# Kernel optimization log

Measured on AMD Instinct MI355X. Metric: run time of the kernel, lower is better.

Reference implementation:

```python
import jax, jax.numpy as jnp
import numpy as np

B, N, C = 2, 10000, 128
NH, NP = 4, 20          # n_heads, n_points (n_levels = 1)
DH = C // NH            # head dim = 32
HW = 100                # spatial shape (100, 100), N = HW*HW


def setup_inputs() -> dict:
    key = jax.random.key(0)
    ks = jax.random.split(key, 12)
    s = 0.05  # small param scale so softmax/linears stay well-conditioned
    return {
        "query": jax.random.normal(ks[0], (B, N, C), jnp.float32),
        "query_pos": jax.random.normal(ks[1], (B, N, C), jnp.float32),
        "W_val": jax.random.normal(ks[2], (C, C), jnp.float32) * s,
        "b_val": jax.random.normal(ks[3], (C,), jnp.float32) * s,
        "W_off": jax.random.normal(ks[4], (NH * NP * 2, C), jnp.float32) * s,
        "b_off": jax.random.normal(ks[5], (NH * NP * 2,), jnp.float32) * s,
        "W_attn": jax.random.normal(ks[6], (NH * NP, C), jnp.float32) * s,
        "b_attn": jax.random.normal(ks[7], (NH * NP,), jnp.float32) * s,
        "W_out1": jax.random.normal(ks[8], (C, C), jnp.float32) * s,
        "b_out1": jax.random.normal(ks[9], (C,), jnp.float32) * s,
        "W_out2": jax.random.normal(ks[10], (C, C), jnp.float32) * s,
        "b_out2": jax.random.normal(ks[11], (C,), jnp.float32) * s,
    }


def _msdeform_forward(query, query_pos, W_val, b_val, W_off, b_off,
                      W_attn, b_attn, W_out1, b_out1, W_out2, b_out2):
    residual = query
    q = query + query_pos  # pos added; value branch also uses q (query.clone())

    # reference points: meshgrid of (z, x) normalized to (0,1), shape (N, 2)
    lin = (jnp.arange(HW, dtype=jnp.float32) + 0.5) / HW
    ref_z, ref_x = jnp.meshgrid(lin, lin, indexing="ij")
    ref = jnp.stack([ref_z.reshape(-1), ref_x.reshape(-1)], axis=-1)  # (N,2)

    # projections
    value = (q @ W_val.T + b_val).reshape(B, N, NH, DH).transpose(0, 2, 1, 3)  # (B,NH,N,DH)
    off = (q @ W_off.T + b_off).reshape(B, N, NH, NP, 2)
    attn = jax.nn.softmax((q @ W_attn.T + b_attn).reshape(B, N, NH, NP), axis=-1)

    # sampling locations in normalized coords; offset normalizer = (W, H) = (100, 100)
    loc = ref[None, :, None, None, :] + off / HW  # (B,N,NH,NP,2)

    # grid_sample bilinear, align_corners=False, zeros padding:
    # pixel coord = loc * size - 0.5
    x = (loc[..., 0] * HW - 0.5).transpose(0, 2, 1, 3)  # (B,NH,N,NP)
    y = (loc[..., 1] * HW - 0.5).transpose(0, 2, 1, 3)
    aw = attn.transpose(0, 2, 1, 3)                     # (B,NH,N,NP)

    x0f = jnp.floor(x); y0f = jnp.floor(y)
    wx1 = x - x0f; wy1 = y - y0f
    wx0 = 1.0 - wx1; wy0 = 1.0 - wy1
    ix0 = x0f.astype(jnp.int32); iy0 = y0f.astype(jnp.int32)
    ix1 = ix0 + 1; iy1 = iy0 + 1

    def gather(ix, iy):
        valid = ((ix >= 0) & (ix < HW) & (iy >= 0) & (iy < HW)).astype(value.dtype)
        idx = jnp.clip(iy, 0, HW - 1) * HW + jnp.clip(ix, 0, HW - 1)  # (B,NH,N,NP)
        g = jnp.take_along_axis(value, idx.reshape(B, NH, N * NP, 1), axis=2)
        return g.reshape(B, NH, N, NP, DH) * valid[..., None]

    sampled = ((wx0 * wy0)[..., None] * gather(ix0, iy0)
               + (wx1 * wy0)[..., None] * gather(ix1, iy0)
               + (wx0 * wy1)[..., None] * gather(ix0, iy1)
               + (wx1 * wy1)[..., None] * gather(ix1, iy1))  # (B,NH,N,NP,DH)

    out = (sampled * aw[..., None]).sum(axis=3)             # (B,NH,N,DH)
    out = out.transpose(0, 2, 1, 3).reshape(B, N, C)
    out = out @ W_out1.T + b_out1   # MSDeformAttn.output_proj
    out = out @ W_out2.T + b_out2   # wrapper output_proj
    return out + residual           # dropout is identity in eval


def reference(query, query_pos, W_val, b_val, W_off, b_off,
              W_attn, b_attn, W_out1, b_out1, W_out2, b_out2):
    return _msdeform_forward(query, query_pos, W_val, b_val, W_off, b_off,
                             W_attn, b_attn, W_out1, b_out1, W_out2, b_out2)
```

## Files before the change

### kernel.cpp

```cpp
#include <hip/hip_runtime.h>
#include <hip/hip_bf16.h>
#include <math.h>

#define NTOK 10000
#define BATCH 2
#define CDIM 128
#define NHEAD 4
#define NPNT 20
#define DHEAD 32
#define HWDIM 100
#define MROWS (BATCH * NTOK)
#define OPAD 384
#define PTOK 8
#define PHALO 4
#define PDIM 16
#define NPATCH 13
#define CELLPAD 40

typedef __attribute__((ext_vector_type(8))) short short8v;
typedef __attribute__((ext_vector_type(4))) short short4v;
typedef __attribute__((ext_vector_type(4))) float f32x4;

__device__ __forceinline__ float asf(unsigned u) {
  union { unsigned u; float f; } c; c.u = u; return c.f;
}

__device__ __forceinline__ void acc_cell(const __hip_bfloat16* p, float w,
                                         f32x4& a0, f32x4& a1) {
  int4 u = *(const int4*)p;
  f32x4 g0, g1;
  g0.x = asf(((unsigned)u.x) << 16); g0.y = asf(((unsigned)u.x) & 0xFFFF0000u);
  g0.z = asf(((unsigned)u.y) << 16); g0.w = asf(((unsigned)u.y) & 0xFFFF0000u);
  g1.x = asf(((unsigned)u.z) << 16); g1.y = asf(((unsigned)u.z) & 0xFFFF0000u);
  g1.z = asf(((unsigned)u.w) << 16); g1.w = asf(((unsigned)u.w) & 0xFFFF0000u);
  a0 += g0 * w;
  a1 += g1 * w;
}

__global__ __launch_bounds__(128) void prep_kernel(
    const float* __restrict__ W_val, const float* __restrict__ b_val,
    const float* __restrict__ W_off, const float* __restrict__ b_off,
    const float* __restrict__ W_attn, const float* __restrict__ b_attn,
    const float* __restrict__ W1, const float* __restrict__ b1,
    const float* __restrict__ W2, const float* __restrict__ b2,
    __hip_bfloat16* __restrict__ Wcat, float* __restrict__ bcat,
    __hip_bfloat16* __restrict__ Wc_bf, float* __restrict__ bc) {
  __shared__ float w2row[128];
  __shared__ float red[128];
  const int blk = blockIdx.x, c = threadIdx.x;
  if (blk < OPAD) {
    float v = 0.f, bv = 0.f;
    if (blk < 128) {
      v = W_val[blk * 128 + c]; bv = b_val[blk];
    } else {
      int h = (blk - 128) >> 6, k = (blk - 128) & 63;
      if (k < 40) { v = W_off[(h * 40 + k) * 128 + c]; bv = b_off[h * 40 + k]; }
      else if (k < 60) { v = W_attn[(h * 20 + k - 40) * 128 + c]; bv = b_attn[h * 20 + k - 40]; }
    }
    Wcat[(size_t)blk * 128 + c] = __float2bfloat16(v);
    if (c == 0) bcat[blk] = bv;
  } else {
    const int o = blk - OPAD;
    w2row[c] = W2[o * 128 + c];
    __syncthreads();
    float acc = 0.f;
    for (int k = 0; k < 128; ++k) acc += w2row[k] * W1[k * 128 + c];
    Wc_bf[(size_t)o * 128 + c] = __float2bfloat16(acc);
    red[c] = w2row[c] * b1[c];
    __syncthreads();
    for (int s = 64; s > 0; s >>= 1) {
      if (c < s) red[c] += red[c + s];
      __syncthreads();
    }
    if (c == 0) bc[o] = b2[o] + red[0];
  }
}

__global__ __launch_bounds__(256) void proj1_kernel(
    const float* __restrict__ query, const float* __restrict__ qpos,
    const __hip_bfloat16* __restrict__ Wcat, const float* __restrict__ bcat,
    __hip_bfloat16* __restrict__ value, __hip_bfloat16* __restrict__ oa) {
  __shared__ __hip_bfloat16 qa[64][128];
  __shared__ __hip_bfloat16 wb[64][128];
  const int t = threadIdx.x;
  const int r0 = blockIdx.x * 64;

#pragma unroll
  for (int i = 0; i < 4; ++i) {
    int lin = t + 256 * i;
    int r = lin >> 4, g = lin & 15;
    int c = g << 3;
    float4 v0 = make_float4(0.f, 0.f, 0.f, 0.f);
    float4 v1 = make_float4(0.f, 0.f, 0.f, 0.f);
    if (r0 + r < MROWS) {
      const float* p = query + (size_t)(r0 + r) * CDIM + c;
      v0 = *(const float4*)p;
      v1 = *(const float4*)(p + 4);
      const float* p2 = qpos + (size_t)(r0 + r) * CDIM + c;
      float4 u0 = *(const float4*)p2;
      float4 u1 = *(const float4*)(p2 + 4);
      v0.x += u0.x; v0.y += u0.y; v0.z += u0.z; v0.w += u0.w;
      v1.x += u1.x; v1.y += u1.y; v1.z += u1.z; v1.w += u1.w;
    }
    __hip_bfloat16* dst = &qa[r][(g ^ (r & 7)) << 3];
    dst[0] = __float2bfloat16(v0.x); dst[1] = __float2bfloat16(v0.y);
    dst[2] = __float2bfloat16(v0.z); dst[3] = __float2bfloat16(v0.w);
    dst[4] = __float2bfloat16(v1.x); dst[5] = __float2bfloat16(v1.y);
    dst[6] = __float2bfloat16(v1.z); dst[7] = __float2bfloat16(v1.w);
  }
  {
    const int ot = blockIdx.y * 192;
#pragma unroll
    for (int i = 0; i < 4; ++i) {
      int lin = t + 256 * i;
      int r = lin >> 4, g = lin & 15;
      short8v w = *(const short8v*)(Wcat + (size_t)(ot + r) * 128 + (g << 3));
      *(short8v*)&wb[r][(g ^ (r & 7)) << 3] = w;
    }
  }
  __syncthreads();

  const int wid = t >> 6;
  const int lane = t & 63;
  const int wr = (wid >> 1) * 32;
  const int wc = (wid & 1) * 32;
  const int lrow = lane & 15;
  const int lk = lane >> 4;

  short8v afr[4][2];
  {
    int ra0 = wr + lrow, ra1 = wr + 16 + lrow;
#pragma unroll
    for (int kk = 0; kk < 4; ++kk) {
      int gb = kk * 4 + lk;
      afr[kk][0] = *(const short8v*)&qa[ra0][(gb ^ (ra0 & 7)) << 3];
      afr[kk][1] = *(const short8v*)&qa[ra1][(gb ^ (ra1 & 7)) << 3];
    }
  }

#pragma unroll
  for (int ti = 0; ti < 3; ++ti) {
    const int ot = blockIdx.y * 192 + ti * 64;

    short8v wreg[4];
    if (ti < 2) {
      const int otn = ot + 64;
#pragma unroll
      for (int i = 0; i < 4; ++i) {
        int lin = t + 256 * i;
        int r = lin >> 4, g = lin & 15;
        wreg[i] = *(const short8v*)(Wcat + (size_t)(otn + r) * 128 + (g << 3));
      }
    }

    f32x4 acc[2][2];
#pragma unroll
    for (int mi = 0; mi < 2; ++mi)
#pragma unroll
      for (int ni = 0; ni < 2; ++ni) acc[mi][ni] = (f32x4)(0.f);

#pragma unroll
    for (int kk = 0; kk < 4; ++kk) {
      const int gb = kk * 4 + lk;
      int rb0 = wc + lrow, rb1 = wc + 16 + lrow;
      short8v b0 = *(const short8v*)&wb[rb0][(gb ^ (rb0 & 7)) << 3];
      short8v b1 = *(const short8v*)&wb[rb1][(gb ^ (rb1 & 7)) << 3];
      acc[0][0] = __builtin_amdgcn_mfma_f32_16x16x32_bf16(afr[kk][0], b0, acc[0][0], 0, 0, 0);
      acc[0][1] = __builtin_amdgcn_mfma_f32_16x16x32_bf16(afr[kk][0], b1, acc[0][1], 0, 0, 0);
      acc[1][0] = __builtin_amdgcn_mfma_f32_16x16x32_bf16(afr[kk][1], b0, acc[1][0], 0, 0, 0);
      acc[1][1] = __builtin_amdgcn_mfma_f32_16x16x32_bf16(afr[kk][1], b1, acc[1][1], 0, 0, 0);
    }

    if (ti < 2) {
      __syncthreads();
#pragma unroll
      for (int i = 0; i < 4; ++i) {
        int lin = t + 256 * i;
        int r = lin >> 4, g = lin & 15;
        *(short8v*)&wb[r][(g ^ (r & 7)) << 3] = wreg[i];
      }
    }

#pragma unroll
    for (int mi = 0; mi < 2; ++mi) {
#pragma unroll
      for (int ni = 0; ni < 2; ++ni) {
#pragma unroll
        for (int reg = 0; reg < 4; ++reg) {
          int r = r0 + wr + mi * 16 + (lane >> 4) * 4 + reg;
          int o = ot + wc + ni * 16 + (lane & 15);
          if (r >= MROWS) continue;
          float v = acc[mi][ni][reg] + bcat[o];
          if (o < 128) {
            int b = r >= NTOK ? 1 : 0;
            int n = r - b * NTOK;
            int h = o >> 5, rem = o & 31;
            value[(((size_t)b * NHEAD + h) * NTOK + n) * 32 + rem] =
                __float2bfloat16(v);
          } else {
            oa[(size_t)r * 256 + (o - 128)] = __float2bfloat16(v);
          }
        }
      }
    }

    if (ti < 2) __syncthreads();
  }
}

__global__ __launch_bounds__(256) void proj2_kernel(
    const __hip_bfloat16* __restrict__ outat,
    const __hip_bfloat16* __restrict__ Wc_bf, const float* __restrict__ bc,
    const float* __restrict__ resid, float* __restrict__ out) {
  __shared__ __hip_bfloat16 qa[64][128];
  __shared__ __hip_bfloat16 wb[64][128];
  const int t = threadIdx.x;
  const int r0 = blockIdx.x * 64;
  const int ot = blockIdx.y * 64;

#pragma unroll
  for (int i = 0; i < 4; ++i) {
    int lin = t + 256 * i;
    int r = lin >> 4, g = lin & 15;
    short8v v = (short8v)(short)0;
    if (r0 + r < MROWS)
      v = *(const short8v*)(outat + (size_t)(r0 + r) * CDIM + (g << 3));
    *(short8v*)&qa[r][(g ^ (r & 7)) << 3] = v;
  }
#pragma unroll
  for (int i = 0; i < 4; ++i) {
    int lin = t + 256 * i;
    int r = lin >> 4, g = lin & 15;
    short8v w = *(const short8v*)(Wc_bf + (size_t)(ot + r) * 128 + (g << 3));
    *(short8v*)&wb[r][(g ^ (r & 7)) << 3] = w;
  }
  __syncthreads();

  const int wid = t >> 6;
  const int lane = t & 63;
  const int wr = (wid >> 1) * 32;
  const int wc = (wid & 1) * 32;
  const int lrow = lane & 15;
  const int lk = lane >> 4;

  f32x4 acc[2][2];
#pragma unroll
  for (int mi = 0; mi < 2; ++mi)
#pragma unroll
    for (int ni = 0; ni < 2; ++ni) acc[mi][ni] = (f32x4)(0.f);

#pragma unroll
  for (int kk = 0; kk < 4; ++kk) {
    const int gb = kk * 4 + lk;
    int ra0 = wr + lrow, ra1 = wr + 16 + lrow;
    int rb0 = wc + lrow, rb1 = wc + 16 + lrow;
    short8v a0 = *(const short8v*)&qa[ra0][(gb ^ (ra0 & 7)) << 3];
    short8v a1 = *(const short8v*)&qa[ra1][(gb ^ (ra1 & 7)) << 3];
    short8v b0 = *(const short8v*)&wb[rb0][(gb ^ (rb0 & 7)) << 3];
    short8v b1 = *(const short8v*)&wb[rb1][(gb ^ (rb1 & 7)) << 3];
    acc[0][0] = __builtin_amdgcn_mfma_f32_16x16x32_bf16(a0, b0, acc[0][0], 0, 0, 0);
    acc[0][1] = __builtin_amdgcn_mfma_f32_16x16x32_bf16(a0, b1, acc[0][1], 0, 0, 0);
    acc[1][0] = __builtin_amdgcn_mfma_f32_16x16x32_bf16(a1, b0, acc[1][0], 0, 0, 0);
    acc[1][1] = __builtin_amdgcn_mfma_f32_16x16x32_bf16(a1, b1, acc[1][1], 0, 0, 0);
  }

#pragma unroll
  for (int mi = 0; mi < 2; ++mi) {
#pragma unroll
    for (int ni = 0; ni < 2; ++ni) {
#pragma unroll
      for (int reg = 0; reg < 4; ++reg) {
        int r = r0 + wr + mi * 16 + (lane >> 4) * 4 + reg;
        int o = ot + wc + ni * 16 + (lane & 15);
        if (r >= MROWS) continue;
        out[(size_t)r * CDIM + o] =
            acc[mi][ni][reg] + bc[o] + resid[(size_t)r * CDIM + o];
      }
    }
  }
}

__global__ __launch_bounds__(256) void sample_kernel(
    const __hip_bfloat16* __restrict__ value,
    const __hip_bfloat16* __restrict__ oa, __hip_bfloat16* __restrict__ outat) {
  const int s = blockIdx.x & 7;
  const int pidx = blockIdx.x >> 3;
  const int PI = pidx % NPATCH, PJ = pidx / NPATCH;
  const int I0 = PI * PTOK, J0 = PJ * PTOK;
  const int b = s >> 2, h = s & 3;

  __shared__ __hip_bfloat16 patch[PDIM * PDIM][CELLPAD];
  const __hip_bfloat16* vglob = value + (size_t)s * NTOK * DHEAD;

  const int dl = threadIdx.x & 3;
  const int tok = threadIdx.x >> 2;
  const int li = tok & 7, lj = tok >> 3;
  const int i = I0 + li, j = J0 + lj;
  const bool tv = (i < HWDIM) && (j < HWDIM);
  const int n = tv ? (i * HWDIM + j) : 0;
  union { int4 v4[8]; unsigned u[32]; } d;
  {
    const int4* p4 =
        (const int4*)(oa + ((size_t)(b * NTOK + n)) * 256 + h * 64);
#pragma unroll
    for (int q = 0; q < 8; ++q) d.v4[q] = p4[q];
  }

#pragma unroll
  for (int it = 0; it < 4; ++it) {
    int lin = threadIdx.x + 256 * it;
    int cell = lin >> 2, part = lin & 3;
    int py = cell >> 4, px = cell & 15;
    int gy = J0 - PHALO + py;
    int gx = I0 - PHALO + px;
    short8v v = (short8v)(short)0;
    if (gy >= 0 && gy < HWDIM && gx >= 0 && gx < HWDIM)
      v = *(const short8v*)(vglob + ((size_t)(gy * HWDIM + gx)) * DHEAD +
                            part * 8);
    *(short8v*)&patch[cell][part * 8] = v;
  }
  __syncthreads();

  if (!tv) return;

  float e[NPNT];
  float ssum = 0.f;
#pragma unroll
  for (int q = 0; q < 10; ++q) {
    unsigned uu = d.u[20 + q];
    float e0 = __expf(asf(uu << 16));
    float e1 = __expf(asf(uu & 0xFFFF0000u));
    e[2 * q] = e0; e[2 * q + 1] = e1;
    ssum += e0 + e1;
  }
  const float inv = 1.f / ssum;

  const float fi = (float)i, fj = (float)j;
  f32x4 c0a = (f32x4)(0.f), c0b = (f32x4)(0.f);
  f32x4 c1a = (f32x4)(0.f), c1b = (f32x4)(0.f);
  f32x4 c2a = (f32x4)(0.f), c2b = (f32x4)(0.f);
  f32x4 c3a = (f32x4)(0.f), c3b = (f32x4)(0.f);
#pragma unroll
  for (int p = 0; p < NPNT; ++p) {
    const unsigned up = d.u[p];
    float x = fi + asf(up << 16);
    float y = fj + asf(up & 0xFFFF0000u);
    float aw = e[p];
    float x0f = floorf(x), y0f = floorf(y);
    int ix0 = (int)x0f, iy0 = (int)y0f;
    float wx1 = x - x0f, wy1 = y - y0f;
    float wx0 = 1.f - wx1, wy0 = 1.f - wy1;
    float wya = aw * wy0, wyb = aw * wy1;
    float w00 = wya * wx0, w01 = wya * wx1;
    float w10 = wyb * wx0, w11 = wyb * wx1;
    int ly = iy0 - (J0 - PHALO);
    int lx = ix0 - (I0 - PHALO);
    if ((unsigned)ly <= PDIM - 2 && (unsigned)lx <= PDIM - 2) {
      const __hip_bfloat16* pb = &patch[ly * PDIM + lx][dl * 8];
      acc_cell(pb, w00, c0a, c0b);
      acc_cell(pb + CELLPAD, w01, c1a, c1b);
      acc_cell(pb + PDIM * CELLPAD, w10, c2a, c2b);
      acc_cell(pb + PDIM * CELLPAD + CELLPAD, w11, c3a, c3b);
    } else {
      float wgt[4] = {w00, w01, w10, w11};
#pragma unroll
      for (int cy = 0; cy < 2; ++cy) {
        int iy = iy0 + cy;
        if (iy < 0 || iy >= HWDIM) continue;
#pragma unroll
        for (int cx = 0; cx < 2; ++cx) {
          int ix = ix0 + cx;
          if (ix < 0 || ix >= HWDIM) continue;
          acc_cell(vglob + ((size_t)(iy * HWDIM + ix)) * DHEAD + dl * 8,
                   wgt[cy * 2 + cx], c0a, c0b);
        }
      }
    }
  }
  f32x4 a0 = (c0a + c1a) + (c2a + c3a);
  f32x4 a1 = (c0b + c1b) + (c2b + c3b);

  union { short8v v8; __hip_bfloat16 hh[8]; } o;
#pragma unroll
  for (int k = 0; k < 4; ++k) {
    o.hh[k] = __float2bfloat16(a0[k] * inv);
    o.hh[4 + k] = __float2bfloat16(a1[k] * inv);
  }
  *(short8v*)(outat + ((size_t)b * NTOK + n) * CDIM + h * DHEAD + dl * 8) =
      o.v8;
}

extern "C" void kernel_launch(void* const* d_in, const int* in_sizes, int n_in,
                              void* d_out, int out_size, void* d_ws,
                              size_t ws_size, hipStream_t stream) {
  const float* query = (const float*)d_in[0];
  const float* query_pos = (const float*)d_in[1];
  const float* W_val = (const float*)d_in[2];
  const float* b_val = (const float*)d_in[3];
  const float* W_off = (const float*)d_in[4];
  const float* b_off = (const float*)d_in[5];
  const float* W_attn = (const float*)d_in[6];
  const float* b_attn = (const float*)d_in[7];
  const float* W_out1 = (const float*)d_in[8];
  const float* b_out1 = (const float*)d_in[9];
  const float* W_out2 = (const float*)d_in[10];
  const float* b_out2 = (const float*)d_in[11];
  float* out = (float*)d_out;

  char* ws = (char*)d_ws;
  __hip_bfloat16* value = (__hip_bfloat16*)ws;
  ws += (size_t)MROWS * CDIM * 2;
  __hip_bfloat16* oa = (__hip_bfloat16*)ws;
  ws += (size_t)MROWS * 256 * 2;
  __hip_bfloat16* outat = (__hip_bfloat16*)ws;
  ws += (size_t)MROWS * CDIM * 2;
  float* bcat = (float*)ws; ws += OPAD * 4;
  float* bc = (float*)ws; ws += 128 * 4;
  __hip_bfloat16* Wcat = (__hip_bfloat16*)ws; ws += (size_t)OPAD * 128 * 2;
  __hip_bfloat16* Wc_bf = (__hip_bfloat16*)ws;

  prep_kernel<<<OPAD + 128, 128, 0, stream>>>(
      W_val, b_val, W_off, b_off, W_attn, b_attn, W_out1, b_out1, W_out2,
      b_out2, Wcat, bcat, Wc_bf, bc);

  proj1_kernel<<<dim3(313, 2), 256, 0, stream>>>(query, query_pos, Wcat, bcat,
                                                 value, oa);

  sample_kernel<<<8 * NPATCH * NPATCH, 256, 0, stream>>>(value, oa, outat);

  proj2_kernel<<<dim3(313, 2), 256, 0, stream>>>(outat, Wc_bf, bc, query, out);
}
```

Before: 59.33 us.

## Split offset/attention buffers into head-major layout with fp32 attention logits

The projection kernel now writes sampling offsets in bf16 and attention logits in fp32 into separate head-major buffers (b, head, token). The sampler then reads a contiguous 80-byte offset record and an 80-byte logit record per token instead of a strided 128-byte slice of a token-major combined buffer, and skips the bf16 unpacking of logits. The proj1 weight double-buffering through registers is dropped in favour of a simple load-sync-compute per tile, which adds barriers and exposes global load latency but lowers register pressure. Keeping the logits in fp32 costs extra bytes written, and the head-major stores from proj1 are more scattered.

```diff
diff --git a/kernel.cpp b/kernel.cpp
--- a/kernel.cpp
+++ b/kernel.cpp
@@ -79,7 +79,8 @@
 __global__ __launch_bounds__(256) void proj1_kernel(
     const float* __restrict__ query, const float* __restrict__ qpos,
     const __hip_bfloat16* __restrict__ Wcat, const float* __restrict__ bcat,
-    __hip_bfloat16* __restrict__ value, __hip_bfloat16* __restrict__ oa) {
+    __hip_bfloat16* __restrict__ value, __hip_bfloat16* __restrict__ offb,
+    float* __restrict__ attnb) {
   __shared__ __hip_bfloat16 qa[64][128];
   __shared__ __hip_bfloat16 wb[64][128];
   const int t = threadIdx.x;
@@ -108,16 +109,6 @@
     dst[4] = __float2bfloat16(v1.x); dst[5] = __float2bfloat16(v1.y);
     dst[6] = __float2bfloat16(v1.z); dst[7] = __float2bfloat16(v1.w);
   }
-  {
-    const int ot = blockIdx.y * 192;
-#pragma unroll
-    for (int i = 0; i < 4; ++i) {
-      int lin = t + 256 * i;
-      int r = lin >> 4, g = lin & 15;
-      short8v w = *(const short8v*)(Wcat + (size_t)(ot + r) * 128 + (g << 3));
-      *(short8v*)&wb[r][(g ^ (r & 7)) << 3] = w;
-    }
-  }
   __syncthreads();
 
   const int wid = t >> 6;
@@ -138,20 +129,17 @@
     }
   }
 
-#pragma unroll
   for (int ti = 0; ti < 3; ++ti) {
     const int ot = blockIdx.y * 192 + ti * 64;
-
-    short8v wreg[4];
-    if (ti < 2) {
-      const int otn = ot + 64;
-#pragma unroll
-      for (int i = 0; i < 4; ++i) {
-        int lin = t + 256 * i;
-        int r = lin >> 4, g = lin & 15;
-        wreg[i] = *(const short8v*)(Wcat + (size_t)(otn + r) * 128 + (g << 3));
-      }
-    }
+    __syncthreads();
+#pragma unroll
+    for (int i = 0; i < 4; ++i) {
+      int lin = t + 256 * i;
+      int r = lin >> 4, g = lin & 15;
+      short8v w = *(const short8v*)(Wcat + (size_t)(ot + r) * 128 + (g << 3));
+      *(short8v*)&wb[r][(g ^ (r & 7)) << 3] = w;
+    }
+    __syncthreads();
 
     f32x4 acc[2][2];
 #pragma unroll
@@ -171,16 +159,6 @@
       acc[1][1] = __builtin_amdgcn_mfma_f32_16x16x32_bf16(afr[kk][1], b1, acc[1][1], 0, 0, 0);
     }
 
-    if (ti < 2) {
-      __syncthreads();
-#pragma unroll
-      for (int i = 0; i < 4; ++i) {
-        int lin = t + 256 * i;
-        int r = lin >> 4, g = lin & 15;
-        *(short8v*)&wb[r][(g ^ (r & 7)) << 3] = wreg[i];
-      }
-    }
-
 #pragma unroll
     for (int mi = 0; mi < 2; ++mi) {
 #pragma unroll
@@ -191,20 +169,24 @@
           int o = ot + wc + ni * 16 + (lane & 15);
           if (r >= MROWS) continue;
           float v = acc[mi][ni][reg] + bcat[o];
+          int b = r >= NTOK ? 1 : 0;
+          int n = r - b * NTOK;
           if (o < 128) {
-            int b = r >= NTOK ? 1 : 0;
-            int n = r - b * NTOK;
             int h = o >> 5, rem = o & 31;
             value[(((size_t)b * NHEAD + h) * NTOK + n) * 32 + rem] =
                 __float2bfloat16(v);
           } else {
-            oa[(size_t)r * 256 + (o - 128)] = __float2bfloat16(v);
+            int h = (o - 128) >> 6, k = (o - 128) & 63;
+            size_t base = ((size_t)(b * NHEAD + h) * NTOK + n);
+            if (k < 40) {
+              offb[base * 40 + k] = __float2bfloat16(v);
+            } else if (k < 60) {
+              attnb[base * 20 + (k - 40)] = v;
+            }
           }
         }
       }
     }
-
-    if (ti < 2) __syncthreads();
   }
 }
 
@@ -282,7 +264,8 @@
 
 __global__ __launch_bounds__(256) void sample_kernel(
     const __hip_bfloat16* __restrict__ value,
-    const __hip_bfloat16* __restrict__ oa, __hip_bfloat16* __restrict__ outat) {
+    const __hip_bfloat16* __restrict__ off, const float* __restrict__ attn,
+    __hip_bfloat16* __restrict__ outat) {
   const int s = blockIdx.x & 7;
   const int pidx = blockIdx.x >> 3;
   const int PI = pidx % NPATCH, PJ = pidx / NPATCH;
@@ -298,12 +281,15 @@
   const int i = I0 + li, j = J0 + lj;
   const bool tv = (i < HWDIM) && (j < HWDIM);
   const int n = tv ? (i * HWDIM + j) : 0;
-  union { int4 v4[8]; unsigned u[32]; } d;
+  union { int4 v4[5]; unsigned u[20]; } of;
+  union { float4 v4[5]; float f[20]; } at;
   {
-    const int4* p4 =
-        (const int4*)(oa + ((size_t)(b * NTOK + n)) * 256 + h * 64);
-#pragma unroll
-    for (int q = 0; q < 8; ++q) d.v4[q] = p4[q];
+    const int4* o4 = (const int4*)(off + ((size_t)s * NTOK + n) * 40);
+    const float4* a4 = (const float4*)(attn + ((size_t)s * NTOK + n) * 20);
+#pragma unroll
+    for (int q = 0; q < 5; ++q) of.v4[q] = o4[q];
+#pragma unroll
+    for (int q = 0; q < 5; ++q) at.v4[q] = a4[q];
   }
 
 #pragma unroll
@@ -323,15 +309,11 @@
 
   if (!tv) return;
 
-  float e[NPNT];
   float ssum = 0.f;
 #pragma unroll
-  for (int q = 0; q < 10; ++q) {
-    unsigned uu = d.u[20 + q];
-    float e0 = __expf(asf(uu << 16));
-    float e1 = __expf(asf(uu & 0xFFFF0000u));
-    e[2 * q] = e0; e[2 * q + 1] = e1;
-    ssum += e0 + e1;
+  for (int p = 0; p < NPNT; ++p) {
+    at.f[p] = __expf(at.f[p]);
+    ssum += at.f[p];
   }
   const float inv = 1.f / ssum;
 
@@ -342,10 +324,10 @@
   f32x4 c3a = (f32x4)(0.f), c3b = (f32x4)(0.f);
 #pragma unroll
   for (int p = 0; p < NPNT; ++p) {
-    const unsigned up = d.u[p];
+    const unsigned up = of.u[p];
     float x = fi + asf(up << 16);
     float y = fj + asf(up & 0xFFFF0000u);
-    float aw = e[p];
+    float aw = at.f[p];
     float x0f = floorf(x), y0f = floorf(y);
     int ix0 = (int)x0f, iy0 = (int)y0f;
     float wx1 = x - x0f, wy1 = y - y0f;
@@ -410,8 +392,10 @@
   char* ws = (char*)d_ws;
   __hip_bfloat16* value = (__hip_bfloat16*)ws;
   ws += (size_t)MROWS * CDIM * 2;
-  __hip_bfloat16* oa = (__hip_bfloat16*)ws;
-  ws += (size_t)MROWS * 256 * 2;
+  __hip_bfloat16* offb = (__hip_bfloat16*)ws;
+  ws += (size_t)MROWS * 160 * 2;
+  float* attnb = (float*)ws;
+  ws += (size_t)MROWS * 80 * 4;
   __hip_bfloat16* outat = (__hip_bfloat16*)ws;
   ws += (size_t)MROWS * CDIM * 2;
   float* bcat = (float*)ws; ws += OPAD * 4;
@@ -424,9 +408,10 @@
       b_out2, Wcat, bcat, Wc_bf, bc);
 
   proj1_kernel<<<dim3(313, 2), 256, 0, stream>>>(query, query_pos, Wcat, bcat,
-                                                 value, oa);
-
-  sample_kernel<<<8 * NPATCH * NPATCH, 256, 0, stream>>>(value, oa, outat);
+                                                 value, offb, attnb);
+
+  sample_kernel<<<8 * NPATCH * NPATCH, 256, 0, stream>>>(value, offb, attnb,
+                                                         outat);
 
   proj2_kernel<<<dim3(313, 2), 256, 0, stream>>>(outat, Wc_bf, bc, query, out);
 }
```

Result: slower. 61.61 us (+3.8%).
